# Kernel tuning notes

Hardware: AMD Instinct MI355X
Metric: run time of the kernel (lower is better)

The kernel has to match this reference:

```python
import jax, jax.numpy as jnp
import numpy as np

BN_EPS = 1e-5
SCI_NOTATION_THRESHOLD = 1e16  # python float repr uses 'e+' only for |v| >= 1e16
NEG_SLOPE = 0.5


def _rescale(x):
    # Mirrors: str(max_abs.item()).split('e+') -> divide by 10**exponent when repr is scientific.
    m = jnp.max(jnp.abs(x))
    exp = jnp.floor(jnp.log10(jnp.maximum(m, 1.0)))
    return jnp.where(m >= SCI_NOTATION_THRESHOLD, x / (10.0 ** exp), x)


def _block(x, w, b, g, beta):
    # Linear (+ rescale), BatchNorm1d training-mode (+ rescale), LeakyReLU(0.5) (+ rescale)
    x = _rescale(x @ w.T + b)
    mu = jnp.mean(x, axis=0)
    var = jnp.mean(jnp.square(x - mu), axis=0)  # biased var, as torch BN normalization
    x = _rescale(g * (x - mu) * jax.lax.rsqrt(var + BN_EPS) + beta)
    x = _rescale(jnp.where(x >= 0, x, NEG_SLOPE * x))
    return x


def _uniform(k, shape, fan_in):
    bound = 1.0 / np.sqrt(fan_in)
    return jax.random.uniform(k, shape, jnp.float32, -bound, bound)


def setup_inputs() -> dict:
    key = jax.random.key(0)
    ks = jax.random.split(key, 9)
    B, D = 32768, 512
    H1, H2, H3, O = 2048, 2048, 1024, 1
    return {
        "x": jax.random.normal(ks[0], (B, D), jnp.float32),
        "w1": _uniform(ks[1], (H1, D), D),
        "b1": _uniform(ks[2], (H1,), D),
        "g1": jnp.ones((H1,), jnp.float32),
        "be1": jnp.zeros((H1,), jnp.float32),
        "w2": _uniform(ks[3], (H2, H1), H1),
        "b2": _uniform(ks[4], (H2,), H1),
        "g2": jnp.ones((H2,), jnp.float32),
        "be2": jnp.zeros((H2,), jnp.float32),
        "w3": _uniform(ks[5], (H3, H2), H2),
        "b3": _uniform(ks[6], (H3,), H2),
        "g3": jnp.ones((H3,), jnp.float32),
        "be3": jnp.zeros((H3,), jnp.float32),
        "wout": _uniform(ks[7], (O, H3), H3),
        "bout": _uniform(ks[8], (O,), H3),
    }


def reference(x, w1, b1, g1, be1, w2, b2, g2, be2, w3, b3, g3, be3, wout, bout):
    x = _block(x, w1, b1, g1, be1)
    x = _block(x, w2, b2, g2, be2)
    x = _block(x, w3, b3, g3, be3)
    return x @ wout.T + bout  # [B, 1]
```

## Files before the change

kernel.cpp:

```cpp
#include <hip/hip_runtime.h>

typedef __bf16 bf16x8 __attribute__((ext_vector_type(8)));
typedef float f32x4 __attribute__((ext_vector_type(4)));
typedef unsigned short us8 __attribute__((ext_vector_type(8)));

typedef __attribute__((address_space(3))) void lds_void_t;
typedef const __attribute__((address_space(1))) void gbl_void_t;

__device__ __forceinline__ unsigned short f2bf(float f) {
    unsigned u = __builtin_bit_cast(unsigned, f);
    u += 0x7FFFu + ((u >> 16) & 1u);
    return (unsigned short)(u >> 16);
}
__device__ __forceinline__ float bf2f(unsigned short h) {
    unsigned u = ((unsigned)h) << 16;
    return __builtin_bit_cast(float, u);
}

__global__ void report_ws(float* out, float v) { out[0] = v; }

__global__ __launch_bounds__(256) void cast_bf16(
    const float* __restrict__ src, unsigned short* __restrict__ dst, size_t n8)
{
    size_t i = (size_t)blockIdx.x * 256 + threadIdx.x;
    if (i >= n8) return;
    const float4* s = (const float4*)src + i * 2;
    float4 a = s[0], b = s[1];
    us8 o;
    o[0] = f2bf(a.x); o[1] = f2bf(a.y); o[2] = f2bf(a.z); o[3] = f2bf(a.w);
    o[4] = f2bf(b.x); o[5] = f2bf(b.y); o[6] = f2bf(b.z); o[7] = f2bf(b.w);
    *((us8*)dst + i) = o;
}


#define LOAD_AQ(QH) \
  _Pragma("unroll") for (int mm = 0; mm < 4; ++mm) \
    _Pragma("unroll") for (int s = 0; s < 2; ++s) \
      aq[mm][s] = *(const bf16x8*)&lds[aoff + ((QH)*64 + mm*16 + fr)*64 + (((s*4 + fq) ^ w7) << 3)];

#define LOAD_BP(G) \
  _Pragma("unroll") for (int nn = 0; nn < 2; ++nn) \
    _Pragma("unroll") for (int s = 0; s < 2; ++s) \
      bq[(G)*2+nn][s] = *(const bf16x8*)&lds[boff + ((wc&1)*64 + ((G)*2+nn)*16 + fr)*64 + (((s*4 + fq) ^ w7) << 3)];

#define MFMA_QUAD(QH, G) \
  _Pragma("unroll") for (int mm = 0; mm < 4; ++mm) \
    _Pragma("unroll") for (int nn = 0; nn < 2; ++nn) \
      _Pragma("unroll") for (int s = 0; s < 2; ++s) \
        acc[(QH)*4+mm][(G)*2+nn] = __builtin_amdgcn_mfma_f32_16x16x32_bf16( \
            aq[mm][s], bq[(G)*2+nn][s], acc[(QH)*4+mm][(G)*2+nn], 0, 0, 0);

__global__ __launch_bounds__(512, 2) void gemm256(
    const unsigned short* __restrict__ A,
    const unsigned short* __restrict__ W,
    const float* __restrict__ bias,
    unsigned short* __restrict__ Y,
    float* __restrict__ psum, float* __restrict__ psumsq,
    int M, int N, int K, int rowBlkBase)
{
    __shared__ unsigned short lds[65536];

    const int nbx = N >> 8;
    const int nwg = gridDim.x;
    const int cpx = nwg >> 3;
    const int bid = blockIdx.x;
    const int swzb = (bid & 7) * cpx + (bid >> 3);
    const int bm = swzb / nbx;
    const int bn = swzb % nbx;

    const int t    = threadIdx.x;
    const int wid  = t >> 6;
    const int lane = t & 63;
    const int wrh  = wid >> 2;
    const int wc   = wid & 3;
    const int fr   = lane & 15;
    const int fq   = lane >> 4;
    const int w7   = fr & 7;

    const int r0s  = t >> 3;
    const int ce   = (((t & 7) ^ ((t >> 3) & 7)) << 3);

    const size_t baseA = (size_t)(bm << 8) * K;
    const size_t baseW = (size_t)(bn << 8) * K;
    const int NT = K >> 6;

    auto STAGE = [&](int b, int op, int h, int kt) {
        const unsigned short* gsrc = (op ? W : A)
            + (op ? baseW : baseA)
            + (size_t)((h << 7) + r0s) * K + (kt << 6) + ce;
        char* dst = (char*)lds + ((((b * 2 + op) * 2 + h) << 14) + (wid << 10));
        __builtin_amdgcn_global_load_lds((gbl_void_t*)gsrc, (lds_void_t*)dst, 16, 0, 0);
        __builtin_amdgcn_global_load_lds((gbl_void_t*)(gsrc + (size_t)64 * K),
                                         (lds_void_t*)(dst + 8192), 16, 0, 0);
    };

    f32x4 acc[8][4];
#pragma unroll
    for (int m = 0; m < 8; ++m)
#pragma unroll
        for (int n = 0; n < 4; ++n)
            acc[m][n] = (f32x4){0.f, 0.f, 0.f, 0.f};

    STAGE(0, 1, 0, 0); STAGE(0, 1, 1, 0);
    STAGE(0, 0, 0, 0); STAGE(0, 0, 1, 0);
    if (NT > 1) { STAGE(1, 1, 0, 1); STAGE(1, 1, 1, 1); }
    asm volatile("s_waitcnt vmcnt(4)" ::: "memory");
    __builtin_amdgcn_s_barrier();

    bf16x8 aq[4][2], bq[4][2];

    for (int kt = 0; kt < NT; ++kt) {
        const int b = kt & 1;
        const unsigned aoff = (unsigned)(b * 4 + wrh) * 8192;
        const unsigned boff = (unsigned)(b * 4 + 2 + (wc >> 1)) * 8192;

        LOAD_AQ(0);
        LOAD_BP(0);
        if (kt + 1 < NT) STAGE(b ^ 1, 0, 0, kt + 1);
        __builtin_amdgcn_s_barrier();
        asm volatile("s_waitcnt lgkmcnt(0)" ::: "memory");
        __builtin_amdgcn_s_setprio(1);
        MFMA_QUAD(0, 0);
        __builtin_amdgcn_s_setprio(0);
        __builtin_amdgcn_s_barrier();

        LOAD_BP(1);
        if (kt + 1 < NT) STAGE(b ^ 1, 0, 1, kt + 1);
        __builtin_amdgcn_s_barrier();
        asm volatile("s_waitcnt lgkmcnt(0)" ::: "memory");
        __builtin_amdgcn_s_setprio(1);
        MFMA_QUAD(0, 1);
        __builtin_amdgcn_s_setprio(0);
        __builtin_amdgcn_s_barrier();

        LOAD_AQ(1);
        if (kt + 2 < NT) STAGE(b, 1, 0, kt + 2);
        __builtin_amdgcn_s_barrier();
        asm volatile("s_waitcnt lgkmcnt(0)" ::: "memory");
        __builtin_amdgcn_s_setprio(1);
        MFMA_QUAD(1, 0);
        __builtin_amdgcn_s_setprio(0);
        __builtin_amdgcn_s_barrier();

        if (kt + 2 < NT) {
            STAGE(b, 1, 1, kt + 2);
            asm volatile("s_waitcnt vmcnt(4)" ::: "memory");
        } else {
            asm volatile("s_waitcnt vmcnt(0)" ::: "memory");
        }
        __builtin_amdgcn_s_barrier();
        __builtin_amdgcn_s_setprio(1);
        MFMA_QUAD(1, 1);
        __builtin_amdgcn_s_setprio(0);
        __builtin_amdgcn_s_barrier();
    }

    float bv[4];
#pragma unroll
    for (int nn = 0; nn < 4; ++nn) bv[nn] = bias[(bn << 8) + wc * 64 + nn * 16 + fr];

    float* sSum = (float*)lds;
    float* sSq  = (float*)lds + 256 * 8;
#pragma unroll
    for (int nn = 0; nn < 4; ++nn) {
        float s = 0.f, q = 0.f;
#pragma unroll
        for (int mm = 0; mm < 8; ++mm)
#pragma unroll
            for (int r = 0; r < 4; ++r) {
                float v = acc[mm][nn][r] + bv[nn];
                s += v; q += v * v;
            }
        const int col = wc * 64 + nn * 16 + fr;
        const int sl  = wrh * 4 + fq;
        sSum[col * 8 + sl] = s;
        sSq [col * 8 + sl] = q;
    }
    __syncthreads();
    if (t < 256) {
        float s = 0.f, q = 0.f;
#pragma unroll
        for (int k = 0; k < 8; ++k) { s += sSum[t * 8 + k]; q += sSq[t * 8 + k]; }
        psum  [(size_t)(rowBlkBase + bm) * N + (bn << 8) + t] = s;
        psumsq[(size_t)(rowBlkBase + bm) * N + (bn << 8) + t] = q;
    }
    __syncthreads();

#pragma unroll
    for (int nn = 0; nn < 4; ++nn) {
        const int col = wc * 64 + nn * 16 + fr;
#pragma unroll
        for (int mm = 0; mm < 8; ++mm) {
            const int row0 = wrh * 128 + mm * 16 + fq * 4;
#pragma unroll
            for (int r = 0; r < 4; ++r)
                lds[(row0 + r) * 256 + col] = f2bf(acc[mm][nn][r] + bv[nn]);
        }
    }
    __syncthreads();

    {
        const size_t outBase = (size_t)(bm << 8) * N + (bn << 8);
#pragma unroll
        for (int i = 0; i < 16; ++i) {
            const int u   = t + i * 512;
            const int row = u >> 5, sl = u & 31;
            us8 v = *(const us8*)&lds[row * 256 + sl * 8];
            *(us8*)&Y[outBase + (size_t)row * N + sl * 8] = v;
        }
    }
}

__global__ __launch_bounds__(256) void col_stats2(
    const float* __restrict__ psum, const float* __restrict__ psumsq,
    const float* __restrict__ g, const float* __restrict__ be,
    float* __restrict__ scale, float* __restrict__ shift,
    int N, int NB, float invM)
{
    const int col = blockIdx.x * 256 + threadIdx.x;
    float s = 0.f, ss = 0.f;
    for (int c = 0; c < NB; ++c) {
        s  += psum  [(size_t)c * N + col];
        ss += psumsq[(size_t)c * N + col];
    }
    float mu  = s * invM;
    float var = ss * invM - mu * mu;
    float a = g[col] * rsqrtf(var + 1e-5f);
    scale[col] = a;
    shift[col] = be[col] - mu * a;
}

__global__ __launch_bounds__(256) void norm_copy(
    const unsigned short* __restrict__ src, unsigned short* __restrict__ dst,
    const float* __restrict__ scale, const float* __restrict__ shift,
    unsigned colMask8, size_t n8)
{
    size_t i = (size_t)blockIdx.x * 256 + threadIdx.x;
    if (i >= n8) return;
    us8 v = *((const us8*)src + i);
    const unsigned c8 = (unsigned)i & colMask8;
    const float4* sc = (const float4*)scale + c8 * 2;
    const float4* sh = (const float4*)shift + c8 * 2;
    float4 s0 = sc[0], s1 = sc[1], h0 = sh[0], h1 = sh[1];
    float xs[8];
    xs[0] = bf2f(v[0]) * s0.x + h0.x;  xs[1] = bf2f(v[1]) * s0.y + h0.y;
    xs[2] = bf2f(v[2]) * s0.z + h0.z;  xs[3] = bf2f(v[3]) * s0.w + h0.w;
    xs[4] = bf2f(v[4]) * s1.x + h1.x;  xs[5] = bf2f(v[5]) * s1.y + h1.y;
    xs[6] = bf2f(v[6]) * s1.z + h1.z;  xs[7] = bf2f(v[7]) * s1.w + h1.w;
    us8 o;
#pragma unroll
    for (int j = 0; j < 8; ++j) {
        float x = xs[j];
        x = (x >= 0.f) ? x : 0.5f * x;
        o[j] = f2bf(x);
    }
    *((us8*)dst + i) = o;
}

__global__ __launch_bounds__(256) void matvec_norm_out(
    const unsigned short* __restrict__ X, const float* __restrict__ scale,
    const float* __restrict__ shift, const float* __restrict__ wvec,
    const float* __restrict__ bout, float* __restrict__ out, int Kd)
{
    const int row  = blockIdx.x * 4 + (threadIdx.x >> 6);
    const int lane = threadIdx.x & 63;
    const unsigned short* xr = X + (size_t)row * Kd;
    float s = 0.f;
    for (int j = lane * 8; j < Kd; j += 512) {
        us8 x = *(const us8*)(xr + j);
        const float4* sc = (const float4*)(scale + j);
        const float4* sh = (const float4*)(shift + j);
        const float4* wv = (const float4*)(wvec + j);
        float4 s0 = sc[0], s1 = sc[1], h0 = sh[0], h1 = sh[1];
        float4 w0 = wv[0], w1 = wv[1];
        float xs[8] = {
            bf2f(x[0]) * s0.x + h0.x, bf2f(x[1]) * s0.y + h0.y,
            bf2f(x[2]) * s0.z + h0.z, bf2f(x[3]) * s0.w + h0.w,
            bf2f(x[4]) * s1.x + h1.x, bf2f(x[5]) * s1.y + h1.y,
            bf2f(x[6]) * s1.z + h1.z, bf2f(x[7]) * s1.w + h1.w };
        float wf[8] = { w0.x, w0.y, w0.z, w0.w, w1.x, w1.y, w1.z, w1.w };
#pragma unroll
        for (int e = 0; e < 8; ++e) {
            float xv = xs[e];
            xv = (xv >= 0.f) ? xv : 0.5f * xv;
            s += xv * wf[e];
        }
    }
#pragma unroll
    for (int off = 32; off > 0; off >>= 1) s += __shfl_down(s, off);
    if (lane == 0) out[row] = s + bout[0];
}

extern "C" void kernel_launch(void* const* d_in, const int* in_sizes, int n_in,
                              void* d_out, int out_size, void* d_ws, size_t ws_size,
                              hipStream_t stream)
{
    const float* x    = (const float*)d_in[0];
    const float* w1   = (const float*)d_in[1];
    const float* b1   = (const float*)d_in[2];
    const float* g1   = (const float*)d_in[3];
    const float* be1  = (const float*)d_in[4];
    const float* w2   = (const float*)d_in[5];
    const float* b2   = (const float*)d_in[6];
    const float* g2   = (const float*)d_in[7];
    const float* be2  = (const float*)d_in[8];
    const float* w3   = (const float*)d_in[9];
    const float* b3   = (const float*)d_in[10];
    const float* g3   = (const float*)d_in[11];
    const float* be3  = (const float*)d_in[12];
    const float* wout = (const float*)d_in[13];
    const float* bout = (const float*)d_in[14];
    float* out = (float*)d_out;

    const int B = 32768, D = 512, H1 = 2048, H2 = 2048, H3 = 1024;
    const int NB = B / 256;
    const int RCH = 8192;

    char* ws = (char*)d_ws;
    size_t off = 0;
    auto alloc = [&](size_t bytes) -> char* {
        char* p = ws + off;
        off += (bytes + 255) & ~(size_t)255;
        return p;
    };
    unsigned short* bufA    = (unsigned short*)alloc((size_t)B * H1 * 2);
    unsigned short* scratch = (unsigned short*)alloc((size_t)RCH * H1 * 2);
    unsigned short* W1b     = (unsigned short*)alloc((size_t)H1 * D * 2);
    unsigned short* W2b     = (unsigned short*)alloc((size_t)H2 * H1 * 2);
    unsigned short* W3b     = (unsigned short*)alloc((size_t)H3 * H2 * 2);
    float* psum   = (float*)alloc((size_t)NB * H1 * 4);
    float* psumsq = (float*)alloc((size_t)NB * H1 * 4);
    float* scale  = (float*)alloc((size_t)H1 * 4);
    float* shift  = (float*)alloc((size_t)H1 * 4);

    if (off > ws_size) {
        report_ws<<<1, 1, 0, stream>>>(out, (float)ws_size);
        return;
    }

    {
        size_t n8;
        n8 = (size_t)B * D / 8;   cast_bf16<<<(unsigned)((n8 + 255) / 256), 256, 0, stream>>>(x,  scratch, n8);
        n8 = (size_t)H1 * D / 8;  cast_bf16<<<(unsigned)((n8 + 255) / 256), 256, 0, stream>>>(w1, W1b, n8);
        n8 = (size_t)H2 * H1 / 8; cast_bf16<<<(unsigned)((n8 + 255) / 256), 256, 0, stream>>>(w2, W2b, n8);
        n8 = (size_t)H3 * H2 / 8; cast_bf16<<<(unsigned)((n8 + 255) / 256), 256, 0, stream>>>(w3, W3b, n8);
    }

    const float invB = 1.0f / (float)B;
    const size_t chunk8 = (size_t)RCH * H1 / 8;

    gemm256<<<(B / 256) * (H1 / 256), 512, 0, stream>>>(
        scratch, W1b, b1, bufA, psum, psumsq, B, H1, D, 0);
    col_stats2<<<H1 / 256, 256, 0, stream>>>(psum, psumsq, g1, be1, scale, shift, H1, NB, invB);

    for (int c = 0; c < B / RCH; ++c) {
        norm_copy<<<(unsigned)(chunk8 / 256), 256, 0, stream>>>(
            bufA + (size_t)c * RCH * H1, scratch, scale, shift, H1 / 8 - 1, chunk8);
        gemm256<<<(RCH / 256) * (H2 / 256), 512, 0, stream>>>(
            scratch, W2b, b2, bufA + (size_t)c * RCH * H1, psum, psumsq,
            RCH, H2, H1, c * (RCH / 256));
    }
    col_stats2<<<H2 / 256, 256, 0, stream>>>(psum, psumsq, g2, be2, scale, shift, H2, NB, invB);

    for (int c = 0; c < B / RCH; ++c) {
        norm_copy<<<(unsigned)(chunk8 / 256), 256, 0, stream>>>(
            bufA + (size_t)c * RCH * H2, scratch, scale, shift, H2 / 8 - 1, chunk8);
        gemm256<<<(RCH / 256) * (H3 / 256), 512, 0, stream>>>(
            scratch, W3b, b3, bufA + (size_t)c * RCH * H3, psum, psumsq,
            RCH, H3, H2, c * (RCH / 256));
    }
    col_stats2<<<H3 / 256, 256, 0, stream>>>(psum, psumsq, g3, be3, scale, shift, H3, NB, invB);

    matvec_norm_out<<<B / 4, 256, 0, stream>>>(bufA, scale, shift, wout, bout, out, H3);
}
```

Baseline: 803.6 us.

## Restage GEMM prefetch pipeline, enlarge chunks, normalize layer-3 input in place

The GEMM prologue and main loop now prefetch both the A and W tiles for step kt+2 together at the end of each iteration, in place of staging A for kt+1 mid-iteration, with matching vmcnt waits. Layer 2 is processed in two larger row chunks. Layer 3 normalizes the full activation buffer in place and runs one full-size GEMM into a new dedicated output buffer. The normalize kernel becomes grid-stride and LeakyReLU uses fmaxf. The aim is fewer launches and fewer GEMM waves, plus better load latency hiding, at the cost of a larger workspace and a changed wait/barrier schedule that risks stalls.

```diff
diff --git a/kernel.cpp b/kernel.cpp
--- a/kernel.cpp
+++ b/kernel.cpp
@@ -101,10 +101,15 @@
         for (int n = 0; n < 4; ++n)
             acc[m][n] = (f32x4){0.f, 0.f, 0.f, 0.f};
 
+    STAGE(0, 0, 0, 0); STAGE(0, 0, 1, 0);
     STAGE(0, 1, 0, 0); STAGE(0, 1, 1, 0);
-    STAGE(0, 0, 0, 0); STAGE(0, 0, 1, 0);
-    if (NT > 1) { STAGE(1, 1, 0, 1); STAGE(1, 1, 1, 1); }
-    asm volatile("s_waitcnt vmcnt(4)" ::: "memory");
+    if (NT > 1) {
+        STAGE(1, 0, 0, 1); STAGE(1, 0, 1, 1);
+        STAGE(1, 1, 0, 1); STAGE(1, 1, 1, 1);
+        asm volatile("s_waitcnt vmcnt(8)" ::: "memory");
+    } else {
+        asm volatile("s_waitcnt vmcnt(0)" ::: "memory");
+    }
     __builtin_amdgcn_s_barrier();
 
     bf16x8 aq[4][2], bq[4][2];
@@ -116,7 +121,7 @@
 
         LOAD_AQ(0);
         LOAD_BP(0);
-        if (kt + 1 < NT) STAGE(b ^ 1, 0, 0, kt + 1);
+        asm volatile("s_waitcnt lgkmcnt(8)" ::: "memory");
         __builtin_amdgcn_s_barrier();
         asm volatile("s_waitcnt lgkmcnt(0)" ::: "memory");
         __builtin_amdgcn_s_setprio(1);
@@ -125,7 +130,6 @@
         __builtin_amdgcn_s_barrier();
 
         LOAD_BP(1);
-        if (kt + 1 < NT) STAGE(b ^ 1, 0, 1, kt + 1);
         __builtin_amdgcn_s_barrier();
         asm volatile("s_waitcnt lgkmcnt(0)" ::: "memory");
         __builtin_amdgcn_s_setprio(1);
@@ -143,8 +147,10 @@
         __builtin_amdgcn_s_barrier();
 
         if (kt + 2 < NT) {
+            STAGE(b, 0, 0, kt + 2);
+            STAGE(b, 0, 1, kt + 2);
             STAGE(b, 1, 1, kt + 2);
-            asm volatile("s_waitcnt vmcnt(4)" ::: "memory");
+            asm volatile("s_waitcnt vmcnt(8)" ::: "memory");
         } else {
             asm volatile("s_waitcnt vmcnt(0)" ::: "memory");
         }
@@ -198,7 +204,6 @@
         }
     }
     __syncthreads();
-
     {
         const size_t outBase = (size_t)(bm << 8) * N + (bn << 8);
 #pragma unroll
@@ -230,31 +235,32 @@
     shift[col] = be[col] - mu * a;
 }
 
-__global__ __launch_bounds__(256) void norm_copy(
+__global__ __launch_bounds__(256) void norm_full(
     const unsigned short* __restrict__ src, unsigned short* __restrict__ dst,
     const float* __restrict__ scale, const float* __restrict__ shift,
     unsigned colMask8, size_t n8)
 {
-    size_t i = (size_t)blockIdx.x * 256 + threadIdx.x;
-    if (i >= n8) return;
-    us8 v = *((const us8*)src + i);
-    const unsigned c8 = (unsigned)i & colMask8;
-    const float4* sc = (const float4*)scale + c8 * 2;
-    const float4* sh = (const float4*)shift + c8 * 2;
-    float4 s0 = sc[0], s1 = sc[1], h0 = sh[0], h1 = sh[1];
-    float xs[8];
-    xs[0] = bf2f(v[0]) * s0.x + h0.x;  xs[1] = bf2f(v[1]) * s0.y + h0.y;
-    xs[2] = bf2f(v[2]) * s0.z + h0.z;  xs[3] = bf2f(v[3]) * s0.w + h0.w;
-    xs[4] = bf2f(v[4]) * s1.x + h1.x;  xs[5] = bf2f(v[5]) * s1.y + h1.y;
-    xs[6] = bf2f(v[6]) * s1.z + h1.z;  xs[7] = bf2f(v[7]) * s1.w + h1.w;
-    us8 o;
-#pragma unroll
-    for (int j = 0; j < 8; ++j) {
-        float x = xs[j];
-        x = (x >= 0.f) ? x : 0.5f * x;
-        o[j] = f2bf(x);
-    }
-    *((us8*)dst + i) = o;
+    const size_t stride = (size_t)gridDim.x * 256;
+    for (size_t i = (size_t)blockIdx.x * 256 + threadIdx.x; i < n8; i += stride) {
+        us8 v = *((const us8*)src + i);
+        const unsigned c8 = (unsigned)i & colMask8;
+        const float4* sc = (const float4*)scale + c8 * 2;
+        const float4* sh = (const float4*)shift + c8 * 2;
+        float4 s0 = sc[0], s1 = sc[1], h0 = sh[0], h1 = sh[1];
+        float xs[8];
+        xs[0] = bf2f(v[0]) * s0.x + h0.x;  xs[1] = bf2f(v[1]) * s0.y + h0.y;
+        xs[2] = bf2f(v[2]) * s0.z + h0.z;  xs[3] = bf2f(v[3]) * s0.w + h0.w;
+        xs[4] = bf2f(v[4]) * s1.x + h1.x;  xs[5] = bf2f(v[5]) * s1.y + h1.y;
+        xs[6] = bf2f(v[6]) * s1.z + h1.z;  xs[7] = bf2f(v[7]) * s1.w + h1.w;
+        us8 o;
+#pragma unroll
+        for (int j = 0; j < 8; ++j) {
+            float x = xs[j];
+            x = fmaxf(x, 0.5f * x);
+            o[j] = f2bf(x);
+        }
+        *((us8*)dst + i) = o;
+    }
 }
 
 __global__ __launch_bounds__(256) void matvec_norm_out(
@@ -282,7 +288,7 @@
 #pragma unroll
         for (int e = 0; e < 8; ++e) {
             float xv = xs[e];
-            xv = (xv >= 0.f) ? xv : 0.5f * xv;
+            xv = fmaxf(xv, 0.5f * xv);
             s += xv * wf[e];
         }
     }
@@ -314,20 +320,21 @@
 
     const int B = 32768, D = 512, H1 = 2048, H2 = 2048, H3 = 1024;
     const int NB = B / 256;
-    const int RCH = 8192;
-
+    const int RCH = 16384;
+    const float invB = 1.0f / (float)B;
     char* ws = (char*)d_ws;
+
     size_t off = 0;
     auto alloc = [&](size_t bytes) -> char* {
         char* p = ws + off;
         off += (bytes + 255) & ~(size_t)255;
         return p;
     };
-    unsigned short* bufA    = (unsigned short*)alloc((size_t)B * H1 * 2);
-    unsigned short* scratch = (unsigned short*)alloc((size_t)RCH * H1 * 2);
-    unsigned short* W1b     = (unsigned short*)alloc((size_t)H1 * D * 2);
-    unsigned short* W2b     = (unsigned short*)alloc((size_t)H2 * H1 * 2);
-    unsigned short* W3b     = (unsigned short*)alloc((size_t)H3 * H2 * 2);
+    unsigned short* bufA  = (unsigned short*)alloc((size_t)B * H1 * 2);
+    unsigned short* bufY3 = (unsigned short*)alloc((size_t)B * H3 * 2);
+    unsigned short* W1b   = (unsigned short*)alloc((size_t)H1 * D * 2);
+    unsigned short* W2b   = (unsigned short*)alloc((size_t)H2 * H1 * 2);
+    unsigned short* W3b   = (unsigned short*)alloc((size_t)H3 * H2 * 2);
     float* psum   = (float*)alloc((size_t)NB * H1 * 4);
     float* psumsq = (float*)alloc((size_t)NB * H1 * 4);
     float* scale  = (float*)alloc((size_t)H1 * 4);
@@ -340,36 +347,30 @@
 
     {
         size_t n8;
-        n8 = (size_t)B * D / 8;   cast_bf16<<<(unsigned)((n8 + 255) / 256), 256, 0, stream>>>(x,  scratch, n8);
+        n8 = (size_t)B * D / 8;   cast_bf16<<<(unsigned)((n8 + 255) / 256), 256, 0, stream>>>(x,  bufY3, n8);
         n8 = (size_t)H1 * D / 8;  cast_bf16<<<(unsigned)((n8 + 255) / 256), 256, 0, stream>>>(w1, W1b, n8);
         n8 = (size_t)H2 * H1 / 8; cast_bf16<<<(unsigned)((n8 + 255) / 256), 256, 0, stream>>>(w2, W2b, n8);
         n8 = (size_t)H3 * H2 / 8; cast_bf16<<<(unsigned)((n8 + 255) / 256), 256, 0, stream>>>(w3, W3b, n8);
     }
 
-    const float invB = 1.0f / (float)B;
+    gemm256<<<(B / 256) * (H1 / 256), 512, 0, stream>>>(
+        bufY3, W1b, b1, bufA, psum, psumsq, B, H1, D, 0);
+    col_stats2<<<H1 / 256, 256, 0, stream>>>(psum, psumsq, g1, be1, scale, shift, H1, NB, invB);
+
     const size_t chunk8 = (size_t)RCH * H1 / 8;
-
-    gemm256<<<(B / 256) * (H1 / 256), 512, 0, stream>>>(
-        scratch, W1b, b1, bufA, psum, psumsq, B, H1, D, 0);
-    col_stats2<<<H1 / 256, 256, 0, stream>>>(psum, psumsq, g1, be1, scale, shift, H1, NB, invB);
-
     for (int c = 0; c < B / RCH; ++c) {
-        norm_copy<<<(unsigned)(chunk8 / 256), 256, 0, stream>>>(
-            bufA + (size_t)c * RCH * H1, scratch, scale, shift, H1 / 8 - 1, chunk8);
+        norm_full<<<2048, 256, 0, stream>>>(
+            bufA + (size_t)c * RCH * H1, bufY3, scale, shift, H1 / 8 - 1, chunk8);
         gemm256<<<(RCH / 256) * (H2 / 256), 512, 0, stream>>>(
-            scratch, W2b, b2, bufA + (size_t)c * RCH * H1, psum, psumsq,
+            bufY3, W2b, b2, bufA + (size_t)c * RCH * H1, psum, psumsq,
             RCH, H2, H1, c * (RCH / 256));
     }
     col_stats2<<<H2 / 256, 256, 0, stream>>>(psum, psumsq, g2, be2, scale, shift, H2, NB, invB);
 
-    for (int c = 0; c < B / RCH; ++c) {
-        norm_copy<<<(unsigned)(chunk8 / 256), 256, 0, stream>>>(
-            bufA + (size_t)c * RCH * H2, scratch, scale, shift, H2 / 8 - 1, chunk8);
-        gemm256<<<(RCH / 256) * (H3 / 256), 512, 0, stream>>>(
-            scratch, W3b, b3, bufA + (size_t)c * RCH * H3, psum, psumsq,
-            RCH, H3, H2, c * (RCH / 256));
-    }
+    norm_full<<<4096, 256, 0, stream>>>(bufA, bufA, scale, shift, H2 / 8 - 1, (size_t)B * H2 / 8);
+    gemm256<<<(B / 256) * (H3 / 256), 512, 0, stream>>>(
+        bufA, W3b, b3, bufY3, psum, psumsq, B, H3, H2, 0);
     col_stats2<<<H3 / 256, 256, 0, stream>>>(psum, psumsq, g3, be3, scale, shift, H3, NB, invB);
 
-    matvec_norm_out<<<B / 4, 256, 0, stream>>>(bufA, scale, shift, wout, bout, out, H3);
-}
+    matvec_norm_out<<<B / 4, 256, 0, stream>>>(bufY3, scale, shift, wout, bout, out, H3);
+}
```

Result: faster. 689.3 us (-14.2%).
